# Optimization experiments

Measured on AMD Instinct MI355X. Metric: run time of the kernel, lower is better.

The kernel has to match this reference:

```python
import jax, jax.numpy as jnp
import numpy as np

EPS = 1e-8

def setup_inputs() -> dict:
    key = jax.random.key(0)
    k1, k2, k3 = jax.random.split(key, 3)
    B, N, C = 4, 2048, 512
    x = jax.random.normal(k1, (B, N, C), dtype=jnp.float32)
    w_qkv = jax.random.normal(k2, (C, 3 * C), dtype=jnp.float32) * (C ** -0.5)
    w_proj = jax.random.normal(k3, (C, C), dtype=jnp.float32) * (C ** -0.5)
    b_proj = jnp.zeros((C,), dtype=jnp.float32)
    alpha = jnp.ones((1,), dtype=jnp.float32)
    beta = jnp.ones((1,), dtype=jnp.float32)
    return {"x": x, "w_qkv": w_qkv, "alpha": alpha, "beta": beta,
            "w_proj": w_proj, "b_proj": b_proj}

def reference(x, w_qkv, alpha, beta, w_proj, b_proj):
    B, N, C = x.shape
    H = 8  # num_heads
    D = C // H  # head_dim = 64
    scale = D ** -0.5
    qkv = (x @ w_qkv).reshape(B, N, 3, H, D)
    q = jnp.transpose(qkv[:, :, 0], (0, 2, 1, 3))  # (B,H,N,D)
    k = jnp.transpose(qkv[:, :, 1], (0, 2, 1, 3))
    v = jnp.transpose(qkv[:, :, 2], (0, 2, 1, 3))
    attn = jnp.einsum('bhnd,bhmd->bhnm', q, k) * scale  # (B,H,N,N)
    # sparse branch: relu^2 sum-normalize
    sp = jnp.square(jax.nn.relu(attn))
    attn_sparse = sp / (sp.sum(axis=-1, keepdims=True) + EPS)
    # dense branch: softmax
    attn_dense = jax.nn.softmax(attn, axis=-1)
    a = jax.nn.sigmoid(alpha)
    b = jax.nn.sigmoid(beta)
    wsum = a + b + EPS
    attn_final = (a / wsum) * attn_sparse + (b / wsum) * attn_dense
    out = jnp.einsum('bhnm,bhmd->bhnd', attn_final, v)  # (B,H,N,D)
    out = jnp.transpose(out, (0, 2, 1, 3)).reshape(B, N, C)
    return out @ w_proj + b_proj
```

## Files before the change

### kernel.cpp

```cpp
#include <hip/hip_runtime.h>

typedef unsigned short u16;
typedef unsigned int   u32;
typedef __attribute__((ext_vector_type(8))) __bf16 bf16x8;
typedef __attribute__((ext_vector_type(4))) float  f32x4;
typedef __attribute__((ext_vector_type(4))) u32    u32x4;

#define AS1q __attribute__((address_space(1)))
#define AS3q __attribute__((address_space(3)))

static __device__ __forceinline__ u16 f2bf(float f) {
    u32 u = __builtin_bit_cast(u32, f);
    u32 r = u + 0x7FFFu + ((u >> 16) & 1u);
    return (u16)(r >> 16);
}

static __device__ __forceinline__ bf16x8 ld16(const u16* p) {
    return __builtin_bit_cast(bf16x8, *(const float4*)(const void*)p);
}

static __device__ __forceinline__ f32x4 mfma16(bf16x8 a, bf16x8 b, f32x4 c) {
    return __builtin_amdgcn_mfma_f32_16x16x32_bf16(a, b, c, 0, 0, 0);
}

static __device__ __forceinline__ void gld16(const u16* g, u16* l) {
    __builtin_amdgcn_global_load_lds((const AS1q u32*)g, (AS3q u32*)l, 16, 0, 0);
}

static __device__ __forceinline__ float exp2_fast(float v) {
    float e;
    asm("v_exp_f32 %0, %1" : "=v"(e) : "v"(v));
    return e;
}

static __device__ __forceinline__ u32 cvtpk(float lo, float hi_) {
    u32 d;
    asm("v_cvt_pk_bf16_f32 %0, %1, %2" : "=v"(d) : "v"(lo), "v"(hi_));
    return d;
}

__global__ __launch_bounds__(256) void k_cast_x(const float* __restrict__ x, u16* __restrict__ xb) {
    int i = blockIdx.x * 256 + threadIdx.x;
    float4 v = ((const float4*)x)[i];
    ushort4 o;
    o.x = f2bf(v.x); o.y = f2bf(v.y); o.z = f2bf(v.z); o.w = f2bf(v.w);
    ((ushort4*)xb)[i] = o;
}

__global__ __launch_bounds__(256) void k_transpose_cast(const float* __restrict__ in, u16* __restrict__ out,
                                                        int K, int Nn) {
    __shared__ float tile[32][33];
    int tx = threadIdx.x & 31, ty = threadIdx.x >> 5;
    int k0 = blockIdx.y * 32, n0 = blockIdx.x * 32;
#pragma unroll
    for (int i = 0; i < 4; ++i)
        tile[ty + i * 8][tx] = in[(k0 + ty + i * 8) * Nn + n0 + tx];
    __syncthreads();
#pragma unroll
    for (int i = 0; i < 4; ++i)
        out[(n0 + ty + i * 8) * K + k0 + tx] = f2bf(tile[tx][ty + i * 8]);
}

static __device__ __forceinline__ void stage128x64(const u16* __restrict__ gbase, int ld,
                                                   u16* lds, int tid) {
    int wid = tid >> 6;
#pragma unroll
    for (int i = 0; i < 4; ++i) {
        int idx = i * 256 + tid;
        int row = idx >> 3, c8 = idx & 7;
        int csw = c8 ^ (row & 7);
        gld16(gbase + row * ld + csw * 8, lds + (i * 256 + wid * 64) * 8);
    }
}

static __device__ __forceinline__ bf16x8 frag(const u16* lds, int row, int col16) {
    return ld16(lds + row * 64 + ((col16 ^ (row & 7)) << 3));
}

__global__ __launch_bounds__(256) void k_gemm_qkv(const u16* __restrict__ xb, const u16* __restrict__ wT,
                                                  u16* __restrict__ Qh, u16* __restrict__ Kh,
                                                  u16* __restrict__ VTh) {
    __shared__ __align__(16) u16 at[128 * 64];
    __shared__ __align__(16) u16 bt[128 * 64];
    int tid = threadIdx.x, lane = tid & 63, wid = tid >> 6;
    int tm = blockIdx.x / 12, tn = blockIdx.x % 12;
    int rb = tm * 128, cb = tn * 128;
    int wr = (wid >> 1) * 64, wc = (wid & 1) * 64;
    int l15 = lane & 15, lhi = lane >> 4;
    f32x4 acc[4][4] = {};
    for (int kk = 0; kk < 512; kk += 64) {
        stage128x64(xb + rb * 512 + kk, 512, at, tid);
        stage128x64(wT + cb * 512 + kk, 512, bt, tid);
        __syncthreads();
        bf16x8 af[4][2], bfr[4][2];
#pragma unroll
        for (int m = 0; m < 4; ++m) {
            int row = wr + m * 16 + l15;
            af[m][0] = frag(at, row, lhi);
            af[m][1] = frag(at, row, 4 + lhi);
        }
#pragma unroll
        for (int n = 0; n < 4; ++n) {
            int row = wc + n * 16 + l15;
            bfr[n][0] = frag(bt, row, lhi);
            bfr[n][1] = frag(bt, row, 4 + lhi);
        }
#pragma unroll
        for (int m = 0; m < 4; ++m)
#pragma unroll
            for (int n = 0; n < 4; ++n) {
                acc[m][n] = mfma16(af[m][0], bfr[n][0], acc[m][n]);
                acc[m][n] = mfma16(af[m][1], bfr[n][1], acc[m][n]);
            }
        __syncthreads();
    }
#pragma unroll
    for (int m = 0; m < 4; ++m)
#pragma unroll
        for (int n = 0; n < 4; ++n)
#pragma unroll
            for (int r = 0; r < 4; ++r) {
                int R  = rb + wr + m * 16 + lhi * 4 + r;
                int Cg = cb + wc + n * 16 + l15;
                int b = R >> 11, nseq = R & 2047;
                int s = Cg >> 9, rm = Cg & 511, h = rm >> 6, d = rm & 63;
                int bh = (b << 3) + h;
                float v = acc[m][n][r];
                if (s == 0)      Qh[(bh * 2048 + nseq) * 64 + d] = f2bf(v * 0.1803368801111244f);
                else if (s == 1) Kh[(bh * 2048 + nseq) * 64 + d] = f2bf(v);
                else             VTh[(bh * 64 + d) * 2048 + nseq] = f2bf(v);
            }
}

#define ATTN_STEP(BUF)                                                           \
    {                                                                            \
        f32x4 s[2][2];                                                           \
        _Pragma("unroll")                                                        \
        for (int kt = 0; kt < 2; ++kt) {                                         \
            int row = kap + 2 * kt;                                              \
            const u16* kbp = &kls[BUF][0] + row * 64;                            \
            bf16x8 kf0 = ld16(kbp + ((lhi ^ (row & 7)) << 3));                   \
            bf16x8 kf1 = ld16(kbp + (((4 + lhi) ^ (row & 7)) << 3));             \
            _Pragma("unroll")                                                    \
            for (int qg = 0; qg < 2; ++qg) {                                     \
                s[qg][kt] = mfma16(kf0, qa[qg][0], z);                           \
                s[qg][kt] = mfma16(kf1, qa[qg][1], s[qg][kt]);                   \
            }                                                                    \
        }                                                                        \
        bf16x8 pfd[2], pfs[2];                                                   \
        _Pragma("unroll")                                                        \
        for (int qg = 0; qg < 2; ++qg) {                                         \
            float ed[2][4], ps[2][4];                                            \
            _Pragma("unroll")                                                    \
            for (int kt = 0; kt < 2; ++kt)                                       \
                _Pragma("unroll")                                                \
                for (int r = 0; r < 4; ++r) {                                    \
                    float v = s[qg][kt][r];                                      \
                    float e = exp2_fast(v);                                      \
                    float t = fmaxf(v, 0.f);                                     \
                    float p = t * t;                                             \
                    dend[qg] += e; dens[qg] += p;                                \
                    ed[kt][r] = e; ps[kt][r] = p;                                \
                }                                                                \
            pfd[qg] = __builtin_bit_cast(bf16x8, (u32x4){                        \
                cvtpk(ed[0][0], ed[0][1]), cvtpk(ed[1][0], ed[1][1]),            \
                cvtpk(ed[0][2], ed[0][3]), cvtpk(ed[1][2], ed[1][3])});          \
            pfs[qg] = __builtin_bit_cast(bf16x8, (u32x4){                        \
                cvtpk(ps[0][0], ps[0][1]), cvtpk(ps[1][0], ps[1][1]),            \
                cvtpk(ps[0][2], ps[0][3]), cvtpk(ps[1][2], ps[1][3])});          \
        }                                                                        \
        _Pragma("unroll")                                                        \
        for (int n = 0; n < 4; ++n) {                                            \
            int row = n * 16 + l15;                                              \
            bf16x8 vf = ld16(&vls[BUF][0] + row * 32 + ((lhi ^ (row & 3)) << 3));\
            _Pragma("unroll")                                                    \
            for (int qg = 0; qg < 2; ++qg) {                                     \
                accd[qg][n] = mfma16(pfd[qg], vf, accd[qg][n]);                  \
                accs[qg][n] = mfma16(pfs[qg], vf, accs[qg][n]);                  \
            }                                                                    \
        }                                                                        \
    }

__global__ __launch_bounds__(256) void k_attn(const u16* __restrict__ Qh, const u16* __restrict__ Kh,
                                              const u16* __restrict__ VTh, const float* __restrict__ alpha,
                                              const float* __restrict__ beta, u16* __restrict__ AO) {
    __shared__ __align__(16) u16 kls[2][32 * 64];
    __shared__ __align__(16) u16 vls[2][64 * 32];
    int tid = threadIdx.x, lane = tid & 63, wid = tid >> 6;
    int l15 = lane & 15, lhi = lane >> 4;
    int wg = (blockIdx.x & 7) * 64 + (blockIdx.x >> 3);
    int bh = wg >> 4;
    int qb = (wg & 15) << 7;
    const u16* Qp = Qh + bh * (2048 * 64);
    const u16* Kp = Kh + bh * (2048 * 64);
    const u16* Vp = VTh + bh * (2048 * 64);
    int qbase = qb + wid * 32;
    bf16x8 qa[2][2];
#pragma unroll
    for (int qg = 0; qg < 2; ++qg) {
        int row = qbase + qg * 16 + l15;
        qa[qg][0] = ld16(Qp + row * 64 + lhi * 8);
        qa[qg][1] = ld16(Qp + row * 64 + 32 + lhi * 8);
    }
    int kap = 8 * (l15 >> 2) + 4 * ((l15 >> 1) & 1) + (l15 & 1);
    f32x4 accd[2][4] = {}, accs[2][4] = {};
    float dend[2] = {}, dens[2] = {};
    const f32x4 z = {0.f, 0.f, 0.f, 0.f};

    int krow = tid >> 3, kc8 = tid & 7;
    int vrow = tid >> 2, vc4 = tid & 3;
    const u16* kg = Kp + krow * 64 + ((kc8 ^ (krow & 7)) << 3);
    const u16* vg = Vp + vrow * 2048 + ((vc4 ^ (vrow & 3)) << 3);

    gld16(kg, &kls[0][0] + tid * 8);
    gld16(vg, &vls[0][0] + tid * 8);
    asm volatile("s_waitcnt vmcnt(0)" ::: "memory");
    __builtin_amdgcn_s_barrier();
    const u16* kgp = kg + 32 * 64;
    const u16* vgp = vg + 32;

    for (int kb = 0; kb < 2048; kb += 64) {
        gld16(kgp, &kls[1][0] + tid * 8);
        gld16(vgp, &vls[1][0] + tid * 8);
        kgp += 32 * 64; vgp += 32;
        asm volatile("s_waitcnt vmcnt(2)" ::: "memory");
        __builtin_amdgcn_s_barrier();
        ATTN_STEP(0)
        asm volatile("" ::: "memory");
        __builtin_amdgcn_s_barrier();
        if (kb + 64 < 2048) {
            gld16(kgp, &kls[0][0] + tid * 8);
            gld16(vgp, &vls[0][0] + tid * 8);
            kgp += 32 * 64; vgp += 32;
            asm volatile("s_waitcnt vmcnt(2)" ::: "memory");
        } else {
            asm volatile("s_waitcnt vmcnt(0)" ::: "memory");
        }
        __builtin_amdgcn_s_barrier();
        ATTN_STEP(1)
        asm volatile("" ::: "memory");
        __builtin_amdgcn_s_barrier();
    }
#pragma unroll
    for (int qg = 0; qg < 2; ++qg) {
        dend[qg] += __shfl_xor(dend[qg], 16); dend[qg] += __shfl_xor(dend[qg], 32);
        dens[qg] += __shfl_xor(dens[qg], 16); dens[qg] += __shfl_xor(dens[qg], 32);
    }
    float sa = 1.f / (1.f + __expf(-alpha[0]));
    float sb = 1.f / (1.f + __expf(-beta[0]));
    float wsum = sa + sb + 1e-8f;
    float wa = sa / wsum, wb = sb / wsum;
    int b = bh >> 3, h = bh & 7;
#pragma unroll
    for (int qg = 0; qg < 2; ++qg) {
        float id[4], isr[4];
#pragma unroll
        for (int r = 0; r < 4; ++r) {
            float dd = __shfl(dend[qg], lhi * 4 + r);
            float ds = __shfl(dens[qg], lhi * 4 + r);
            id[r] = wb / dd;
            isr[r] = wa / (ds + 1e-8f);
        }
#pragma unroll
        for (int n = 0; n < 4; ++n)
#pragma unroll
            for (int r = 0; r < 4; ++r) {
                int R  = b * 2048 + qbase + qg * 16 + lhi * 4 + r;
                int Cg = h * 64 + n * 16 + l15;
                float o = isr[r] * accs[qg][n][r] + id[r] * accd[qg][n][r];
                AO[R * 512 + Cg] = f2bf(o);
            }
    }
}

__global__ __launch_bounds__(256) void k_gemm_proj(const u16* __restrict__ AO, const u16* __restrict__ wT,
                                                   const float* __restrict__ bproj, float* __restrict__ out) {
    __shared__ __align__(16) u16 at[128 * 64];
    __shared__ __align__(16) u16 bt[128 * 64];
    int tid = threadIdx.x, lane = tid & 63, wid = tid >> 6;
    int tm = blockIdx.x >> 2, tn = blockIdx.x & 3;
    int rb = tm * 128, cb = tn * 128;
    int wr = (wid >> 1) * 64, wc = (wid & 1) * 64;
    int l15 = lane & 15, lhi = lane >> 4;
    f32x4 acc[4][4] = {};
    for (int kk = 0; kk < 512; kk += 64) {
        stage128x64(AO + rb * 512 + kk, 512, at, tid);
        stage128x64(wT + cb * 512 + kk, 512, bt, tid);
        __syncthreads();
        bf16x8 af[4][2], bfr[4][2];
#pragma unroll
        for (int m = 0; m < 4; ++m) {
            int row = wr + m * 16 + l15;
            af[m][0] = frag(at, row, lhi);
            af[m][1] = frag(at, row, 4 + lhi);
        }
#pragma unroll
        for (int n = 0; n < 4; ++n) {
            int row = wc + n * 16 + l15;
            bfr[n][0] = frag(bt, row, lhi);
            bfr[n][1] = frag(bt, row, 4 + lhi);
        }
#pragma unroll
        for (int m = 0; m < 4; ++m)
#pragma unroll
            for (int n = 0; n < 4; ++n) {
                acc[m][n] = mfma16(af[m][0], bfr[n][0], acc[m][n]);
                acc[m][n] = mfma16(af[m][1], bfr[n][1], acc[m][n]);
            }
        __syncthreads();
    }
#pragma unroll
    for (int m = 0; m < 4; ++m)
#pragma unroll
        for (int n = 0; n < 4; ++n)
#pragma unroll
            for (int r = 0; r < 4; ++r) {
                int R  = rb + wr + m * 16 + lhi * 4 + r;
                int Cg = cb + wc + n * 16 + l15;
                out[R * 512 + Cg] = acc[m][n][r] + bproj[Cg];
            }
}

extern "C" void kernel_launch(void* const* d_in, const int* in_sizes, int n_in,
                              void* d_out, int out_size, void* d_ws, size_t ws_size,
                              hipStream_t stream) {
    const float* x      = (const float*)d_in[0];
    const float* w_qkv  = (const float*)d_in[1];
    const float* alpha  = (const float*)d_in[2];
    const float* beta   = (const float*)d_in[3];
    const float* w_proj = (const float*)d_in[4];
    const float* b_proj = (const float*)d_in[5];
    float* out = (float*)d_out;
    char* w = (char*)d_ws;
    u16* xb     = (u16*)(w);
    u16* wqkvT  = (u16*)(w + 8388608);
    u16* wprojT = (u16*)(w + 9961472);
    u16* Qh     = (u16*)(w + 10485760);
    u16* Kh     = (u16*)(w + 18874368);
    u16* VTh    = (u16*)(w + 27262976);
    u16* AO     = xb;

    k_cast_x<<<dim3(4096), dim3(256), 0, stream>>>(x, xb);
    k_transpose_cast<<<dim3(48, 16), dim3(256), 0, stream>>>(w_qkv, wqkvT, 512, 1536);
    k_transpose_cast<<<dim3(16, 16), dim3(256), 0, stream>>>(w_proj, wprojT, 512, 512);
    k_gemm_qkv<<<dim3(768), dim3(256), 0, stream>>>(xb, wqkvT, Qh, Kh, VTh);
    k_attn<<<dim3(512), dim3(256), 0, stream>>>(Qh, Kh, VTh, alpha, beta, AO);
    k_gemm_proj<<<dim3(256), dim3(256), 0, stream>>>(AO, wprojT, b_proj, out);
}
```

Measured before the change: 143.4 us.

## Merge prep kernels into one launch and raise wave priority around attention MFMAs

Folds the x cast and the two weight transpose-casts into a single kernel, choosing the work by block index, so two kernel launches and the gaps between them disappear. Separately, it wraps the QK and PV MFMA sections of the attention step in s_setprio(1)/s_setprio(0), so waves issuing matrix work are favoured over waves doing the exp/relu math. The prep fusion saves only launch overhead, and the priority hints may or may not improve interleaving on the MI355X scheduler.

After: 139.3 us. -2.8%, faster.

```diff
diff --git a/kernel.cpp b/kernel.cpp
--- a/kernel.cpp
+++ b/kernel.cpp
@@ -39,19 +39,31 @@
     return d;
 }
 
-__global__ __launch_bounds__(256) void k_cast_x(const float* __restrict__ x, u16* __restrict__ xb) {
-    int i = blockIdx.x * 256 + threadIdx.x;
-    float4 v = ((const float4*)x)[i];
-    ushort4 o;
-    o.x = f2bf(v.x); o.y = f2bf(v.y); o.z = f2bf(v.z); o.w = f2bf(v.w);
-    ((ushort4*)xb)[i] = o;
-}
-
-__global__ __launch_bounds__(256) void k_transpose_cast(const float* __restrict__ in, u16* __restrict__ out,
-                                                        int K, int Nn) {
+__global__ __launch_bounds__(256) void k_prep(const float* __restrict__ x, u16* __restrict__ xb,
+                                              const float* __restrict__ wqkv, u16* __restrict__ wqkvT,
+                                              const float* __restrict__ wproj, u16* __restrict__ wprojT) {
     __shared__ float tile[32][33];
-    int tx = threadIdx.x & 31, ty = threadIdx.x >> 5;
-    int k0 = blockIdx.y * 32, n0 = blockIdx.x * 32;
+    int bid = blockIdx.x, tid = threadIdx.x;
+    if (bid < 4096) {
+        int i = bid * 256 + tid;
+        float4 v = ((const float4*)x)[i];
+        ushort4 o;
+        o.x = f2bf(v.x); o.y = f2bf(v.y); o.z = f2bf(v.z); o.w = f2bf(v.w);
+        ((ushort4*)xb)[i] = o;
+        return;
+    }
+    const float* in; u16* out; int K, Nn, bx, by;
+    if (bid < 4864) {
+        int b2 = bid - 4096;
+        in = wqkv; out = wqkvT; K = 512; Nn = 1536;
+        bx = b2 % 48; by = b2 / 48;
+    } else {
+        int b3 = bid - 4864;
+        in = wproj; out = wprojT; K = 512; Nn = 512;
+        bx = b3 % 16; by = b3 / 16;
+    }
+    int tx = tid & 31, ty = tid >> 5;
+    int k0 = by * 32, n0 = bx * 32;
 #pragma unroll
     for (int i = 0; i < 4; ++i)
         tile[ty + i * 8][tx] = in[(k0 + ty + i * 8) * Nn + n0 + tx];
@@ -135,6 +147,7 @@
 #define ATTN_STEP(BUF)                                                           \
     {                                                                            \
         f32x4 s[2][2];                                                           \
+        __builtin_amdgcn_s_setprio(1);                                           \
         _Pragma("unroll")                                                        \
         for (int kt = 0; kt < 2; ++kt) {                                         \
             int row = kap + 2 * kt;                                              \
@@ -147,6 +160,7 @@
                 s[qg][kt] = mfma16(kf1, qa[qg][1], s[qg][kt]);                   \
             }                                                                    \
         }                                                                        \
+        __builtin_amdgcn_s_setprio(0);                                           \
         bf16x8 pfd[2], pfs[2];                                                   \
         _Pragma("unroll")                                                        \
         for (int qg = 0; qg < 2; ++qg) {                                         \
@@ -169,6 +183,7 @@
                 cvtpk(ps[0][0], ps[0][1]), cvtpk(ps[1][0], ps[1][1]),            \
                 cvtpk(ps[0][2], ps[0][3]), cvtpk(ps[1][2], ps[1][3])});          \
         }                                                                        \
+        __builtin_amdgcn_s_setprio(1);                                           \
         _Pragma("unroll")                                                        \
         for (int n = 0; n < 4; ++n) {                                            \
             int row = n * 16 + l15;                                              \
@@ -179,6 +194,7 @@
                 accs[qg][n] = mfma16(pfs[qg], vf, accs[qg][n]);                  \
             }                                                                    \
         }                                                                        \
+        __builtin_amdgcn_s_setprio(0);                                           \
     }
 
 __global__ __launch_bounds__(256) void k_attn(const u16* __restrict__ Qh, const u16* __restrict__ Kh,
@@ -340,9 +356,7 @@
     u16* VTh    = (u16*)(w + 27262976);
     u16* AO     = xb;
 
-    k_cast_x<<<dim3(4096), dim3(256), 0, stream>>>(x, xb);
-    k_transpose_cast<<<dim3(48, 16), dim3(256), 0, stream>>>(w_qkv, wqkvT, 512, 1536);
-    k_transpose_cast<<<dim3(16, 16), dim3(256), 0, stream>>>(w_proj, wprojT, 512, 512);
+    k_prep<<<dim3(5120), dim3(256), 0, stream>>>(x, xb, w_qkv, wqkvT, w_proj, wprojT);
     k_gemm_qkv<<<dim3(768), dim3(256), 0, stream>>>(xb, wqkvT, Qh, Kh, VTh);
     k_attn<<<dim3(512), dim3(256), 0, stream>>>(Qh, Kh, VTh, alpha, beta, AO);
     k_gemm_proj<<<dim3(256), dim3(256), 0, stream>>>(AO, wprojT, b_proj, out);
```
